# Kernel optimization log

Hardware: AMD Instinct MI355X
Metric: run time of the kernel (lower is better)

## Reference

```python
import jax, jax.numpy as jnp
import numpy as np

N_NODES = 20000
N_EDGES = 160000
N_GRAPHS = 64
IN_DIM = 1304  # 1280 + 24
NEG_SLOPE = 0.2


def gat_conv(x, src, dst, W, a_src, a_dst, b, heads, out_ch):
    """PyG-style GATConv (source_to_target flow, self loops already appended).
    x: [N, in], W: [in, heads*out], a_src/a_dst: [heads, out], b: [heads*out].
    Returns [N, heads*out] (concat=True)."""
    N = x.shape[0]
    h = (x @ W).reshape(N, heads, out_ch)                 # [N, H, C]
    e_src = jnp.sum(h * a_src[None], axis=-1)             # [N, H]
    e_dst = jnp.sum(h * a_dst[None], axis=-1)             # [N, H]
    e = jax.nn.leaky_relu(e_src[src] + e_dst[dst], NEG_SLOPE)  # [E, H]
    # softmax over incoming edges of each destination node
    e_max = jax.ops.segment_max(e, dst, num_segments=N)   # [N, H]
    e_exp = jnp.exp(e - e_max[dst])
    denom = jax.ops.segment_sum(e_exp, dst, num_segments=N)
    alpha = e_exp / (denom[dst] + 1e-16)                  # [E, H]
    msg = h[src] * alpha[:, :, None]                      # [E, H, C]
    out = jax.ops.segment_sum(msg, dst, num_segments=N)   # [N, H, C]
    return out.reshape(N, heads * out_ch) + b


def setup_inputs() -> dict:
    key = jax.random.key(0)
    ks = jax.random.split(key, 20)
    x = jax.random.normal(ks[0], (N_NODES, IN_DIM), dtype=jnp.float32)
    edge_index = jax.random.randint(ks[1], (2, N_EDGES), 0, N_NODES, dtype=jnp.int32)
    phy = jax.random.normal(ks[2], (N_GRAPHS, 188), dtype=jnp.float32)
    batch = jnp.sort(jax.random.randint(ks[3], (N_NODES,), 0, N_GRAPHS, dtype=jnp.int32))

    def glorot(k, shape):
        fan_in, fan_out = shape[0], shape[-1]
        lim = jnp.sqrt(6.0 / (fan_in + fan_out))
        return jax.random.uniform(k, shape, jnp.float32, -lim, lim)

    params = {
        # conv1: GATConv(1304, 256, heads=3)
        "W1": glorot(ks[4], (IN_DIM, 3 * 256)),
        "a_src1": glorot(ks[5], (3, 256)) * 0.1,
        "a_dst1": glorot(ks[6], (3, 256)) * 0.1,
        "b1": jnp.zeros((3 * 256,), jnp.float32),
        # conv2: GATConv(768, 256, heads=1)
        "W2": glorot(ks[7], (3 * 256, 256)),
        "a_src2": glorot(ks[8], (1, 256)) * 0.1,
        "a_dst2": glorot(ks[9], (1, 256)) * 0.1,
        "b2": jnp.zeros((256,), jnp.float32),
        # fc1
        "fc1_w1": glorot(ks[10], (188, 128)), "fc1_b1": jnp.zeros((128,), jnp.float32),
        "fc1_w2": glorot(ks[11], (128, 128)), "fc1_b2": jnp.zeros((128,), jnp.float32),
        # fc2
        "fc2_w1": glorot(ks[12], (256 + 128, 192)), "fc2_b1": jnp.zeros((192,), jnp.float32),
        "fc2_w2": glorot(ks[13], (192, 2)), "fc2_b2": jnp.zeros((2,), jnp.float32),
    }
    return {"x": x, "edge_index": edge_index, "phy": phy, "batch": batch, **params}


def reference(x, edge_index, phy, batch,
              W1, a_src1, a_dst1, b1,
              W2, a_src2, a_dst2, b2,
              fc1_w1, fc1_b1, fc1_w2, fc1_b2,
              fc2_w1, fc2_b1, fc2_w2, fc2_b2):
    N = x.shape[0]
    # add self loops (PyG GATConv default)
    loops = jnp.arange(N, dtype=edge_index.dtype)
    src = jnp.concatenate([edge_index[0], loops])
    dst = jnp.concatenate([edge_index[1], loops])

    h = gat_conv(x, src, dst, W1, a_src1, a_dst1, b1, heads=3, out_ch=256)
    h = jax.nn.relu(h)  # dropout is identity at inference
    h = gat_conv(h, src, dst, W2, a_src2, a_dst2, b2, heads=1, out_ch=256)

    # global mean pool per graph
    sums = jax.ops.segment_sum(h, batch, num_segments=N_GRAPHS)        # [B, 256]
    cnts = jax.ops.segment_sum(jnp.ones((N,), h.dtype), batch, num_segments=N_GRAPHS)
    pooled = sums / jnp.maximum(cnts, 1.0)[:, None]

    mid = jax.nn.relu(phy @ fc1_w1 + fc1_b1)
    mid = jax.nn.relu(mid @ fc1_w2 + fc1_b2)

    z = jnp.concatenate([pooled, mid], axis=1)                          # [B, 384]
    z = jax.nn.relu(z @ fc2_w1 + fc2_b1)
    logits = z @ fc2_w2 + fc2_b2
    return jax.nn.softmax(logits, axis=1)
```

## Files before the change

### kernel.cpp

```cpp
#include <hip/hip_runtime.h>
#include <hip/hip_bf16.h>
#include <math.h>

#define NN    20000
#define MP1   20224
#define NP    20096
#define E0    160000
#define EL    180000
#define NG    64
#define INDIM 1304
#define K1P   1344
#define GNT   21
#define GNX   3
#define GMB   79
#define NWG1  (GMB * GNX)
#define FB    ((EL + 511) / 512)
#define NEG_SLOPE 0.2f
#define NSB   20
#define PCH   32

#define ZB    80
#define XB    13272
#define WB    4800

typedef __bf16 bf16x8 __attribute__((ext_vector_type(8)));
typedef __bf16 bf16x4 __attribute__((ext_vector_type(4)));
typedef float  f32x4  __attribute__((ext_vector_type(4)));

__device__ __forceinline__ void gload16(const void* g, void* l) {
    __builtin_amdgcn_global_load_lds(
        (const __attribute__((address_space(1))) void*)g,
        (__attribute__((address_space(3))) void*)l, 16, 0, 0);
}

#define BAR()  { __builtin_amdgcn_s_barrier(); asm volatile("" ::: "memory"); }
#define VMW(n) { asm volatile("s_waitcnt vmcnt(" #n ")" ::: "memory"); __builtin_amdgcn_sched_barrier(0); }

__global__ __launch_bounds__(256)
void init_kernel(uint4* __restrict__ zreg, int n16,
                 const float* __restrict__ X, __hip_bfloat16* __restrict__ Xb,
                 const float* __restrict__ W1, const float* __restrict__ W2,
                 __hip_bfloat16* __restrict__ w1t, __hip_bfloat16* __restrict__ w2t) {
    const int b = blockIdx.x, t = threadIdx.x;
    if (b < ZB) {
        int i = b * 256 + t;
        if (i < n16) zreg[i] = (uint4){0u, 0u, 0u, 0u};
        return;
    }
    if (b < ZB + XB) {
        int idx = (b - ZB) * 256 + t;
        const int nb = K1P / 8;
        int row = idx / nb;
        int cb = (idx - row * nb) * 8;
        union { __hip_bfloat16 h[8]; float4 f4; } u;
        if (row < NN && cb + 8 <= INDIM) {
            const float4* p = (const float4*)(X + (size_t)row * INDIM + cb);
            float4 u0 = p[0], u1 = p[1];
            u.h[0] = __float2bfloat16(u0.x); u.h[1] = __float2bfloat16(u0.y);
            u.h[2] = __float2bfloat16(u0.z); u.h[3] = __float2bfloat16(u0.w);
            u.h[4] = __float2bfloat16(u1.x); u.h[5] = __float2bfloat16(u1.y);
            u.h[6] = __float2bfloat16(u1.z); u.h[7] = __float2bfloat16(u1.w);
        } else {
#pragma unroll
            for (int e = 0; e < 8; e++) {
                float f = (row < NN && cb + e < INDIM) ? X[(size_t)row * INDIM + cb + e] : 0.f;
                u.h[e] = __float2bfloat16(f);
            }
        }
        *(float4*)(Xb + (size_t)row * K1P + cb) = u.f4;
        return;
    }
    {
        int idx = (b - ZB - XB) * 256 + t;
        const int n1 = 768 * K1P;
        if (idx < n1) {
            int n = idx / K1P, k = idx - n * K1P;
            float f = (k < INDIM) ? W1[(size_t)k * 768 + n] : 0.f;
            w1t[idx] = __float2bfloat16(f);
        } else {
            int i2 = idx - n1;
            if (i2 < 256 * 768) {
                int n = i2 / 768, k = i2 - n * 768;
                w2t[i2] = __float2bfloat16(W2[(size_t)k * 256 + n]);
            }
        }
    }
}

__device__ __forceinline__ void stA(const __hip_bfloat16* __restrict__ A, int bm, int kt, int mh,
                                    char* abuf, int w, int l) {
#pragma unroll
    for (int u = 0; u < 2; u++) {
        int rl = (w << 3) + (l >> 3);
        int lrow = u * 128 + mh * 64 + rl;
        int skb = ((l & 7) << 4) ^ ((rl & 7) << 4);
        const char* g = (const char*)(A + (size_t)(bm + lrow) * K1P + kt * 64) + skb;
        gload16(g, abuf + (u * 128 + mh * 64) * 128 + (w << 10));
    }
}

__device__ __forceinline__ void stB(const __hip_bfloat16* __restrict__ Bt, int bn, int kt, int nh,
                                    char* bbuf, int w, int l) {
#pragma unroll
    for (int u = 0; u < 2; u++) {
        int c = u * 2 + (w >> 2);
        int row0 = c * 64 + nh * 32;
        int rl = ((w & 3) << 3) + (l >> 3);
        int skb = ((l & 7) << 4) ^ ((rl & 7) << 4);
        const char* g = (const char*)(Bt + (size_t)(bn + row0 + rl) * K1P + kt * 64) + skb;
        gload16(g, bbuf + row0 * 128 + ((w & 3) << 10));
    }
}

__global__ __launch_bounds__(512)
void gemm256(const __hip_bfloat16* __restrict__ A,
             const __hip_bfloat16* __restrict__ Bt,
             __hip_bfloat16* __restrict__ C,
             const float* __restrict__ a_src, const float* __restrict__ a_dst,
             float* __restrict__ esrc, float* __restrict__ edst, int M,
             const int* __restrict__ ei, const int* __restrict__ off,
             int* __restrict__ cur, int* __restrict__ csr) {
    __shared__ char lds[131072];
    const int t = threadIdx.x;

    if (blockIdx.x >= NWG1) {
        int e = (blockIdx.x - NWG1) * 512 + t;
        if (e < EL) {
            int d = (e < E0) ? ei[E0 + e] : (e - E0);
            int s = (e < E0) ? ei[e] : (e - E0);
            int pos = off[d] + atomicAdd(&cur[d], 1);
            csr[pos] = s;
        }
        return;
    }

    const int w = t >> 6, l = t & 63;
    const int wm = w >> 2, wn = w & 3;
    const int fr = l & 15, fq = l >> 4;
    const int amask = (fr & 7) << 4;

    const int nwg = NWG1;
    const int q8 = nwg >> 3, r8 = nwg & 7;
    const int xcd = blockIdx.x & 7, sub = blockIdx.x >> 3;
    const int logical = (xcd < r8 ? xcd * (q8 + 1) : r8 * (q8 + 1) + (xcd - r8) * q8) + sub;
    const int bm = (logical / GNX) * 256;
    const int bn = (logical % GNX) * 256;

    f32x4 acc[8][4];
#pragma unroll
    for (int i = 0; i < 8; i++)
#pragma unroll
        for (int j = 0; j < 4; j++) acc[i][j] = (f32x4){0.f, 0.f, 0.f, 0.f};

    char* A0 = lds;            char* B0 = lds + 32768;
    char* A1 = lds + 65536;    char* B1 = lds + 98304;

    stA(A, bm, 0, 0, A0, w, l);
    stB(Bt, bn, 0, 0, B0, w, l);
    stA(A, bm, 0, 1, A0, w, l);
    stB(Bt, bn, 0, 1, B0, w, l);
    stA(A, bm, 1, 0, A1, w, l);
    stB(Bt, bn, 1, 0, B1, w, l);
    VMW(8);
    BAR();

    for (int kt = 0; kt < GNT; kt++) {
        char* Ab = lds + (kt & 1) * 65536;
        char* Bb = Ab + 32768;
        char* An = lds + ((kt + 1) & 1) * 65536;
        char* Bn = An + 32768;
        bf16x8 a_c[4][2], b_c0[2][2], b_c1[2][2];

#pragma unroll
        for (int im = 0; im < 4; im++)
#pragma unroll
            for (int kk = 0; kk < 2; kk++)
                a_c[im][kk] = *(const bf16x8*)(Ab + (wm * 128 + im * 16 + fr) * 128 + ((kk * 64 + fq * 16) ^ amask));
#pragma unroll
        for (int jn = 0; jn < 2; jn++)
#pragma unroll
            for (int kk = 0; kk < 2; kk++)
                b_c0[jn][kk] = *(const bf16x8*)(Bb + (wn * 64 + jn * 16 + fr) * 128 + ((kk * 64 + fq * 16) ^ amask));
        if (kt + 1 < GNT) stA(A, bm, kt + 1, 1, An, w, l);
        BAR();
        __builtin_amdgcn_s_setprio(1);
#pragma unroll
        for (int im = 0; im < 4; im++)
#pragma unroll
            for (int jn = 0; jn < 2; jn++)
#pragma unroll
                for (int kk = 0; kk < 2; kk++)
                    acc[im][jn] = __builtin_amdgcn_mfma_f32_16x16x32_bf16(a_c[im][kk], b_c0[jn][kk], acc[im][jn], 0, 0, 0);
        __builtin_amdgcn_s_setprio(0);
        if (kt == GNT - 1) { VMW(0); } else { VMW(6); }
        BAR();

#pragma unroll
        for (int jn = 0; jn < 2; jn++)
#pragma unroll
            for (int kk = 0; kk < 2; kk++)
                b_c1[jn][kk] = *(const bf16x8*)(Bb + (wn * 64 + 32 + jn * 16 + fr) * 128 + ((kk * 64 + fq * 16) ^ amask));
        if (kt + 1 < GNT) stB(Bt, bn, kt + 1, 1, Bn, w, l);
        BAR();
        __builtin_amdgcn_s_setprio(1);
#pragma unroll
        for (int im = 0; im < 4; im++)
#pragma unroll
            for (int jn = 0; jn < 2; jn++)
#pragma unroll
                for (int kk = 0; kk < 2; kk++)
                    acc[im][2 + jn] = __builtin_amdgcn_mfma_f32_16x16x32_bf16(a_c[im][kk], b_c1[jn][kk], acc[im][2 + jn], 0, 0, 0);
        __builtin_amdgcn_s_setprio(0);
        if (kt == GNT - 1) { VMW(2); } else { VMW(10); }
        BAR();

#pragma unroll
        for (int im = 0; im < 4; im++)
#pragma unroll
            for (int kk = 0; kk < 2; kk++)
                a_c[im][kk] = *(const bf16x8*)(Ab + (wm * 128 + 64 + im * 16 + fr) * 128 + ((kk * 64 + fq * 16) ^ amask));
        if (kt + 2 < GNT) stA(A, bm, kt + 2, 0, Ab, w, l);
        BAR();
        __builtin_amdgcn_s_setprio(1);
#pragma unroll
        for (int im = 0; im < 4; im++)
#pragma unroll
            for (int jn = 0; jn < 2; jn++)
#pragma unroll
                for (int kk = 0; kk < 2; kk++)
                    acc[4 + im][jn] = __builtin_amdgcn_mfma_f32_16x16x32_bf16(a_c[im][kk], b_c0[jn][kk], acc[4 + im][jn], 0, 0, 0);
        __builtin_amdgcn_s_setprio(0);
        BAR();

        if (kt + 2 < GNT) stB(Bt, bn, kt + 2, 0, Bb, w, l);
        BAR();
        __builtin_amdgcn_s_setprio(1);
#pragma unroll
        for (int im = 0; im < 4; im++)
#pragma unroll
            for (int jn = 0; jn < 2; jn++)
#pragma unroll
                for (int kk = 0; kk < 2; kk++)
                    acc[4 + im][2 + jn] = __builtin_amdgcn_mfma_f32_16x16x32_bf16(a_c[im][kk], b_c1[jn][kk], acc[4 + im][2 + jn], 0, 0, 0);
        __builtin_amdgcn_s_setprio(0);
        if (kt + 2 < GNT) { VMW(8); }
        else if (kt + 2 == GNT) { VMW(4); }
        BAR();
    }

#pragma unroll
    for (int i = 0; i < 8; i++)
#pragma unroll
        for (int j = 0; j < 4; j++)
#pragma unroll
            for (int r = 0; r < 4; r++) {
                int row = bm + wm * 128 + i * 16 + fq * 4 + r;
                int col = bn + wn * 64 + j * 16 + fr;
                if (row < M) C[(size_t)row * 768 + col] = __float2bfloat16(acc[i][j][r]);
            }

    const int head = bn >> 8;
    float asv[4], adv[4];
#pragma unroll
    for (int j = 0; j < 4; j++) {
        asv[j] = a_src[head * 256 + wn * 64 + j * 16 + fr];
        adv[j] = a_dst[head * 256 + wn * 64 + j * 16 + fr];
    }
    __syncthreads();
    float* eb = (float*)lds;
#pragma unroll
    for (int i = 0; i < 8; i++) {
#pragma unroll
        for (int r = 0; r < 4; r++) {
            float ps = 0.f, pd = 0.f;
#pragma unroll
            for (int j = 0; j < 4; j++) { ps += acc[i][j][r] * asv[j]; pd += acc[i][j][r] * adv[j]; }
#pragma unroll
            for (int o = 8; o >= 1; o >>= 1) { ps += __shfl_xor(ps, o, 64); pd += __shfl_xor(pd, o, 64); }
            if (fr == 0) {
                int rowl = wm * 128 + i * 16 + fq * 4 + r;
                eb[(rowl * 4 + wn) * 2 + 0] = ps;
                eb[(rowl * 4 + wn) * 2 + 1] = pd;
            }
        }
    }
    __syncthreads();
    if (t < 256) {
        int row = bm + t;
        if (row < M) {
            float s = eb[t * 8 + 0] + eb[t * 8 + 2] + eb[t * 8 + 4] + eb[t * 8 + 6];
            float d = eb[t * 8 + 1] + eb[t * 8 + 3] + eb[t * 8 + 5] + eb[t * 8 + 7];
            esrc[row * 3 + head] = s;
            edst[row * 3 + head] = d;
        }
    }
}

__global__ __launch_bounds__(256)
void gemm2_fused(const __hip_bfloat16* __restrict__ A,
                 const __hip_bfloat16* __restrict__ Bt,
                 __hip_bfloat16* __restrict__ C,
                 const float* __restrict__ a_src2, const float* __restrict__ a_dst2,
                 float* __restrict__ esrc, float* __restrict__ edst,
                 int M, int N, int K, int NX) {
    __shared__ __hip_bfloat16 As[2][128 * 32];
    __shared__ __hip_bfloat16 Bs[2][128 * 32];
    const int t = threadIdx.x;
    const int w = t >> 6;
    const int l = t & 63;

    const int nwg = gridDim.x;
    const int q = nwg >> 3, r = nwg & 7;
    const int xcd = blockIdx.x & 7, idx = blockIdx.x >> 3;
    const int logical = (xcd < r ? xcd * (q + 1) : r * (q + 1) + (xcd - r) * q) + idx;
    const int bm = (logical / NX) * 128;
    const int bn = (logical % NX) * 128;

    const int wm = (w >> 1) * 64;
    const int wn = (w & 1) * 64;

    f32x4 acc[4][4];
#pragma unroll
    for (int i = 0; i < 4; i++)
#pragma unroll
        for (int j = 0; j < 4; j++) acc[i][j] = (f32x4){0.f, 0.f, 0.f, 0.f};

    const int sr = t >> 2;
    const int sc = (t & 3) * 8;
    const __hip_bfloat16* a0 = A  + (size_t)(bm + sr)      * K + sc;
    const __hip_bfloat16* a1 = A  + (size_t)(bm + 64 + sr) * K + sc;
    const __hip_bfloat16* b0 = Bt + (size_t)(bn + sr)      * K + sc;
    const __hip_bfloat16* b1 = Bt + (size_t)(bn + 64 + sr) * K + sc;

    const int fr = l & 15;
    const int fq = l >> 4;
    const int NT = K / 32;

    auto stage = [&](int k0, int b) {
        char* asb = (char*)&As[b][0];
        char* bsb = (char*)&Bs[b][0];
        gload16(a0 + k0, asb + w * 1024);
        gload16(a1 + k0, asb + 4096 + w * 1024);
        gload16(b0 + k0, bsb + w * 1024);
        gload16(b1 + k0, bsb + 4096 + w * 1024);
    };

    stage(0, 0);
    __syncthreads();

    for (int kt = 0; kt < NT; kt++) {
        const int cb = kt & 1;
        if (kt + 1 < NT) stage((kt + 1) * 32, cb ^ 1);
        bf16x8 av[4], bv[4];
#pragma unroll
        for (int i = 0; i < 4; i++)
            av[i] = *(const bf16x8*)&As[cb][(wm + i * 16 + fr) * 32 + fq * 8];
#pragma unroll
        for (int j = 0; j < 4; j++)
            bv[j] = *(const bf16x8*)&Bs[cb][(wn + j * 16 + fr) * 32 + fq * 8];
#pragma unroll
        for (int i = 0; i < 4; i++)
#pragma unroll
            for (int j = 0; j < 4; j++)
                acc[i][j] = __builtin_amdgcn_mfma_f32_16x16x32_bf16(av[i], bv[j], acc[i][j], 0, 0, 0);
        __syncthreads();
    }

#pragma unroll
    for (int i = 0; i < 4; i++) {
#pragma unroll
        for (int j = 0; j < 4; j++) {
#pragma unroll
            for (int r2 = 0; r2 < 4; r2++) {
                int row = bm + wm + i * 16 + fq * 4 + r2;
                int col = bn + wn + j * 16 + fr;
                if (row < M) C[(size_t)row * N + col] = __float2bfloat16(acc[i][j][r2]);
            }
        }
    }

    float asv[4], adv[4];
#pragma unroll
    for (int j = 0; j < 4; j++) {
        asv[j] = a_src2[bn + wn + j * 16 + fr];
        adv[j] = a_dst2[bn + wn + j * 16 + fr];
    }
    __syncthreads();
    float* eb = (float*)&As[0][0];
#pragma unroll
    for (int i = 0; i < 4; i++) {
#pragma unroll
        for (int r2 = 0; r2 < 4; r2++) {
            float ps = 0.f, pd = 0.f;
#pragma unroll
            for (int j = 0; j < 4; j++) { ps += acc[i][j][r2] * asv[j]; pd += acc[i][j][r2] * adv[j]; }
#pragma unroll
            for (int o = 8; o >= 1; o >>= 1) { ps += __shfl_xor(ps, o, 64); pd += __shfl_xor(pd, o, 64); }
            if (fr == 0) {
                int rowl = wm + i * 16 + fq * 4 + r2;
                int wnIdx = wn >> 6;
                eb[(rowl * 2 + wnIdx) * 2 + 0] = ps;
                eb[(rowl * 2 + wnIdx) * 2 + 1] = pd;
            }
        }
    }
    __syncthreads();
    if (t < 128) {
        int row = bm + t;
        if (row < M) {
            atomicAdd(&esrc[row], eb[t * 4 + 0] + eb[t * 4 + 2]);
            atomicAdd(&edst[row], eb[t * 4 + 1] + eb[t * 4 + 3]);
        }
    }
}

__global__ void hist_kernel(const int* __restrict__ ei, int* __restrict__ deg) {
    int e = blockIdx.x * 256 + threadIdx.x;
    if (e >= EL) return;
    int d = (e < E0) ? ei[E0 + e] : (e - E0);
    atomicAdd(&deg[d], 1);
}

__global__ __launch_bounds__(1024)
void scan_blk(const int* __restrict__ deg, int* __restrict__ off, int* __restrict__ bsum) {
    __shared__ int wsum[16];
    const int b = blockIdx.x, t = threadIdx.x, lane = t & 63, wv = t >> 6;
    const int i = b * 1024 + t;
    int v = (i < NN) ? deg[i] : 0;
    int x = v;
#pragma unroll
    for (int o = 1; o < 64; o <<= 1) {
        int y = __shfl_up(x, o, 64);
        if (lane >= o) x += y;
    }
    if (lane == 63) wsum[wv] = x;
    __syncthreads();
    if (wv == 0 && lane < 16) {
        int s = wsum[lane];
#pragma unroll
        for (int o = 1; o < 16; o <<= 1) {
            int y = __shfl_up(s, o, 64);
            if (lane >= o) s += y;
        }
        wsum[lane] = s;
    }
    __syncthreads();
    int woff = (wv == 0) ? 0 : wsum[wv - 1];
    if (i < NN) off[i + 1] = woff + x;
    if (t == 1023) bsum[b] = wsum[15];
}

__global__ __launch_bounds__(1024)
void scan_add(int* __restrict__ off, const int* __restrict__ bsum) {
    __shared__ int boffs[NSB];
    const int b = blockIdx.x, t = threadIdx.x;
    if (t < 64) {
        int lane = t;
        int v = (lane < NSB) ? bsum[lane] : 0;
        int x = v;
#pragma unroll
        for (int o = 1; o < 64; o <<= 1) {
            int y = __shfl_up(x, o, 64);
            if (lane >= o) x += y;
        }
        if (lane < NSB) boffs[lane] = x - v;
    }
    __syncthreads();
    const int i = b * 1024 + t;
    if (i < NN) off[i + 1] += boffs[b];
    if (b == 0 && t == 0) off[0] = 0;
}

template<int H, bool RELU, typename OutT>
__global__ __launch_bounds__(256)
void gat_aggregate(const __hip_bfloat16* __restrict__ hfeat,
                   const float* __restrict__ esrc,
                   const float* __restrict__ edst,
                   const int* __restrict__ off, const int* __restrict__ csr,
                   const float* __restrict__ bias,
                   OutT* __restrict__ out, int N) {
    const int wv = threadIdx.x >> 6, lane = threadIdx.x & 63;
    const int n = blockIdx.x * 4 + wv;
    if (n >= N) return;
    const int beg = off[n];
    const int deg = off[n + 1] - beg;

    float ed[H], m[H], den[H];
    f32x4 acc[H];
#pragma unroll
    for (int h = 0; h < H; h++) {
        ed[h] = edst[n * H + h];
        m[h] = -INFINITY;
        den[h] = 0.f;
        acc[h] = (f32x4){0.f, 0.f, 0.f, 0.f};
    }

    for (int base = 0; base < deg; base += 64) {
        const int i = base + lane;
        int s = 0;
        float lg[H];
        if (i < deg) {
            s = csr[beg + i];
#pragma unroll
            for (int h = 0; h < H; h++) {
                float v = esrc[s * H + h] + ed[h];
                lg[h] = (v >= 0.f) ? v : NEG_SLOPE * v;
            }
        } else {
#pragma unroll
            for (int h = 0; h < H; h++) lg[h] = -INFINITY;
        }
        float cm[H];
#pragma unroll
        for (int h = 0; h < H; h++) {
            cm[h] = lg[h];
#pragma unroll
            for (int o = 1; o < 64; o <<= 1)
                cm[h] = fmaxf(cm[h], __shfl_xor(cm[h], o, 64));
        }
#pragma unroll
        for (int h = 0; h < H; h++) {
            float nm = fmaxf(m[h], cm[h]);
            float sc = expf(m[h] - nm);
            den[h] *= sc;
#pragma unroll
            for (int e = 0; e < 4; e++) acc[h][e] *= sc;
            m[h] = nm;
        }
        float wgt[H];
#pragma unroll
        for (int h = 0; h < H; h++) {
            wgt[h] = (i < deg) ? expf(lg[h] - m[h]) : 0.f;
            den[h] += wgt[h];
        }
        const int cnt = min(64, deg - base);
        for (int j = 0; j < cnt; j++) {
            int sj = __shfl(s, j, 64);
#pragma unroll
            for (int h = 0; h < H; h++) {
                float wj = __shfl(wgt[h], j, 64);
                bf16x4 hv = *(const bf16x4*)(hfeat + (size_t)sj * (H * 256) + h * 256 + 4 * lane);
#pragma unroll
                for (int e = 0; e < 4; e++) acc[h][e] += wj * (float)hv[e];
            }
        }
    }
#pragma unroll
    for (int h = 0; h < H; h++) {
#pragma unroll
        for (int o = 1; o < 64; o <<= 1) den[h] += __shfl_xor(den[h], o, 64);
    }
#pragma unroll
    for (int h = 0; h < H; h++) {
        float inv = 1.f / (den[h] + 1e-16f);
        if constexpr (sizeof(OutT) == 2) {
            bf16x4 r;
#pragma unroll
            for (int e = 0; e < 4; e++) {
                float f = acc[h][e] * inv + bias[h * 256 + 4 * lane + e];
                if (RELU) f = fmaxf(f, 0.f);
                r[e] = (__bf16)f;
            }
            *(bf16x4*)((__hip_bfloat16*)out + (size_t)n * (H * 256) + h * 256 + 4 * lane) = r;
        } else {
            float4 r;
            float* rp = &r.x;
#pragma unroll
            for (int e = 0; e < 4; e++) {
                float f = acc[h][e] * inv + bias[h * 256 + 4 * lane + e];
                if (RELU) f = fmaxf(f, 0.f);
                rp[e] = f;
            }
            *(float4*)((float*)out + (size_t)n * (H * 256) + h * 256 + 4 * lane) = r;
        }
    }
}

__device__ __forceinline__ int lower_bound_batch(const int* __restrict__ batch, int key) {
    int lo = 0, hi = NN;
    while (lo < hi) {
        int mid = (lo + hi) >> 1;
        if (batch[mid] < key) lo = mid + 1; else hi = mid;
    }
    return lo;
}

__global__ __launch_bounds__(256)
void pool_partial(const __hip_bfloat16* __restrict__ out2, const int* __restrict__ batch,
                  float* __restrict__ partial, float* __restrict__ cnts) {
    const int g = blockIdx.x, c = blockIdx.y, t = threadIdx.x;
    const int s = lower_bound_batch(batch, g);
    const int e = lower_bound_batch(batch, g + 1);
    float a0 = 0.f, a1 = 0.f, a2 = 0.f, a3 = 0.f;
    int n = s + c;
    for (; n + 3 * PCH < e; n += 4 * PCH) {
        float v0 = __bfloat162float(out2[(size_t)n * 256 + t]);
        float v1 = __bfloat162float(out2[(size_t)(n + PCH) * 256 + t]);
        float v2 = __bfloat162float(out2[(size_t)(n + 2 * PCH) * 256 + t]);
        float v3 = __bfloat162float(out2[(size_t)(n + 3 * PCH) * 256 + t]);
        a0 += v0; a1 += v1; a2 += v2; a3 += v3;
    }
    for (; n < e; n += PCH) a0 += __bfloat162float(out2[(size_t)n * 256 + t]);
    partial[((size_t)g * PCH + c) * 256 + t] = a0 + a1 + a2 + a3;
    if (t == 0 && c == 0) cnts[g] = (float)(e - s);
}

__global__ __launch_bounds__(256)
void head_kernel(const float* __restrict__ partial, const float* __restrict__ cnts,
                 const float* __restrict__ phy,
                 const float* __restrict__ w11, const float* __restrict__ b11,
                 const float* __restrict__ w12, const float* __restrict__ b12,
                 const float* __restrict__ w21, const float* __restrict__ b21,
                 const float* __restrict__ w22, const float* __restrict__ b22,
                 float* __restrict__ out) {
    int g = blockIdx.x, t = threadIdx.x;
    __shared__ float ph[188];
    __shared__ float z[384];
    __shared__ float mid[128];
    __shared__ float t1[192];
    __shared__ float lg[2];
    if (t < 188) ph[t] = phy[g * 188 + t];
    {
        float s = 0.f;
#pragma unroll
        for (int c = 0; c < PCH; c++) s += partial[((size_t)g * PCH + c) * 256 + t];
        z[t] = s / fmaxf(cnts[g], 1.0f);
    }
    __syncthreads();
    if (t < 128) {
        float sm = b11[t];
        for (int k = 0; k < 188; k++) sm += ph[k] * w11[k * 128 + t];
        mid[t] = fmaxf(sm, 0.f);
    }
    __syncthreads();
    if (t < 128) {
        float sm = b12[t];
        for (int k = 0; k < 128; k++) sm += mid[k] * w12[k * 128 + t];
        z[256 + t] = fmaxf(sm, 0.f);
    }
    __syncthreads();
    if (t < 192) {
        float sm = b21[t];
        for (int k = 0; k < 384; k++) sm += z[k] * w21[k * 192 + t];
        t1[t] = fmaxf(sm, 0.f);
    }
    __syncthreads();
    if (t < 2) {
        float sm = b22[t];
        for (int k = 0; k < 192; k++) sm += t1[k] * w22[k * 2 + t];
        lg[t] = sm;
    }
    __syncthreads();
    if (t == 0) {
        float mx = fmaxf(lg[0], lg[1]);
        float e0 = expf(lg[0] - mx), e1 = expf(lg[1] - mx);
        float d = e0 + e1;
        out[g * 2 + 0] = e0 / d;
        out[g * 2 + 1] = e1 / d;
    }
}

extern "C" void kernel_launch(void* const* d_in, const int* in_sizes, int n_in,
                              void* d_out, int out_size, void* d_ws, size_t ws_size,
                              hipStream_t stream) {
    const float* x       = (const float*)d_in[0];
    const int*   ei      = (const int*)  d_in[1];
    const float* phy     = (const float*)d_in[2];
    const int*   batch   = (const int*)  d_in[3];
    const float* W1      = (const float*)d_in[4];
    const float* a_src1  = (const float*)d_in[5];
    const float* a_dst1  = (const float*)d_in[6];
    const float* b1      = (const float*)d_in[7];
    const float* W2      = (const float*)d_in[8];
    const float* a_src2  = (const float*)d_in[9];
    const float* a_dst2  = (const float*)d_in[10];
    const float* b2      = (const float*)d_in[11];
    const float* fc1_w1  = (const float*)d_in[12];
    const float* fc1_b1  = (const float*)d_in[13];
    const float* fc1_w2  = (const float*)d_in[14];
    const float* fc1_b2  = (const float*)d_in[15];
    const float* fc2_w1  = (const float*)d_in[16];
    const float* fc2_b1  = (const float*)d_in[17];
    const float* fc2_w2  = (const float*)d_in[18];
    const float* fc2_b2  = (const float*)d_in[19];
    float* out = (float*)d_out;

    char* base = (char*)d_ws;
    size_t o = 0;
    auto alloc = [&](size_t bytes) { size_t r = o; o += (bytes + 255) & ~255ULL; return r; };

    size_t o_xb   = alloc((size_t)MP1 * K1P * 2);
    size_t o_w1t  = alloc((size_t)768 * K1P * 2);
    size_t o_w2t  = alloc((size_t)256 * 768 * 2);
    size_t o_h1b  = alloc((size_t)NP * 768 * 2);
    size_t o_hob  = alloc((size_t)NP * 768 * 2);
    size_t o_es1  = alloc((size_t)NN * 3 * 4);
    size_t o_ed1  = alloc((size_t)NN * 3 * 4);
    size_t o_es2  = alloc((size_t)NN * 4);
    size_t o_ed2  = alloc((size_t)NN * 4);
    size_t o_deg  = alloc((size_t)(NN + 1) * 4);
    size_t o_cur  = alloc((size_t)NN * 4);
    size_t o_zend = o;
    size_t o_off  = alloc((size_t)(NN + 1) * 4);
    size_t o_csr  = alloc((size_t)EL * 4);
    size_t o_bsum = alloc((size_t)NSB * 4);
    size_t o_part = alloc((size_t)NG * PCH * 256 * 4);
    size_t o_cnts = alloc((size_t)NG * 4);

    __hip_bfloat16* xb   = (__hip_bfloat16*)(base + o_xb);
    __hip_bfloat16* w1t  = (__hip_bfloat16*)(base + o_w1t);
    __hip_bfloat16* w2t  = (__hip_bfloat16*)(base + o_w2t);
    __hip_bfloat16* h1b  = (__hip_bfloat16*)(base + o_h1b);
    __hip_bfloat16* hob  = (__hip_bfloat16*)(base + o_hob);
    __hip_bfloat16* h2b  = (__hip_bfloat16*)(base + o_xb);
    __hip_bfloat16* out2 = (__hip_bfloat16*)(base + o_xb + (size_t)24 * 1024 * 1024);
    float* es1   = (float*)(base + o_es1);
    float* ed1   = (float*)(base + o_ed1);
    float* es2   = (float*)(base + o_es2);
    float* ed2   = (float*)(base + o_ed2);
    int*   deg   = (int*)(base + o_deg);
    int*   cur   = (int*)(base + o_cur);
    int*   offs  = (int*)(base + o_off);
    int*   csr   = (int*)(base + o_csr);
    int*   bsum  = (int*)(base + o_bsum);
    float* part  = (float*)(base + o_part);
    float* cnts  = (float*)(base + o_cnts);

    {
        int n16 = (int)((o_zend - o_es2) / 16);
        init_kernel<<<ZB + XB + WB, 256, 0, stream>>>((uint4*)(base + o_es2), n16,
                                                      x, xb, W1, W2, w1t, w2t);
    }

    hist_kernel<<<(EL + 255) / 256, 256, 0, stream>>>(ei, deg);
    scan_blk<<<NSB, 1024, 0, stream>>>(deg, offs, bsum);
    scan_add<<<NSB, 1024, 0, stream>>>(offs, bsum);

    gemm256<<<NWG1 + FB, 512, 0, stream>>>(xb, w1t, h1b, a_src1, a_dst1, es1, ed1, NN,
                                           ei, offs, cur, csr);
    gat_aggregate<3, true, __hip_bfloat16><<<(NN + 3) / 4, 256, 0, stream>>>(h1b, es1, ed1, offs, csr, b1, hob, NN);

    gemm2_fused<<<2 * 157, 256, 0, stream>>>(hob, w2t, h2b, a_src2, a_dst2, es2, ed2, NN, 256, 768, 2);
    gat_aggregate<1, false, __hip_bfloat16><<<(NN + 3) / 4, 256, 0, stream>>>(h2b, es2, ed2, offs, csr, b2, out2, NN);

    pool_partial<<<dim3(NG, PCH), 256, 0, stream>>>(out2, batch, part, cnts);
    head_kernel<<<NG, 256, 0, stream>>>(part, cnts, phy,
                                        fc1_w1, fc1_b1, fc1_w2, fc1_b2,
                                        fc2_w1, fc2_b1, fc2_w2, fc2_b2, out);
}
```

Measured before the change: 234.6 us.

## Split GAT aggregation across heads and shrink CSR fill blocks to grid-stride

The aggregation kernel now gives each wavefront one (node, head) pair instead of one node handling all heads, so the first layer launches three times as many waves. Each wave carries less register state and the per-head gather chains become independent, which should improve latency hiding. The trade-off is that the CSR index loads, the softmax reductions and the pair division are now repeated once per head. Separately, the CSR fill blocks appended to the first GEMM drop from about 352 to 19 and use a grid-stride loop, so fewer extra workgroups compete with the GEMM tiles.

```diff
diff --git a/kernel.cpp b/kernel.cpp
--- a/kernel.cpp
+++ b/kernel.cpp
@@ -14,7 +14,7 @@
 #define GNX   3
 #define GMB   79
 #define NWG1  (GMB * GNX)
-#define FB    ((EL + 511) / 512)
+#define FB    19
 #define NEG_SLOPE 0.2f
 #define NSB   20
 #define PCH   32
@@ -124,8 +124,7 @@
     const int t = threadIdx.x;
 
     if (blockIdx.x >= NWG1) {
-        int e = (blockIdx.x - NWG1) * 512 + t;
-        if (e < EL) {
+        for (int e = (blockIdx.x - NWG1) * 512 + t; e < EL; e += FB * 512) {
             int d = (e < E0) ? ei[E0 + e] : (e - E0);
             int s = (e < E0) ? ei[e] : (e - E0);
             int pos = off[d] + atomicAdd(&cur[d], 1);
@@ -480,99 +479,70 @@
                    const float* __restrict__ bias,
                    OutT* __restrict__ out, int N) {
     const int wv = threadIdx.x >> 6, lane = threadIdx.x & 63;
-    const int n = blockIdx.x * 4 + wv;
-    if (n >= N) return;
+    const int pair = blockIdx.x * 4 + wv;
+    if (pair >= N * H) return;
+    const int n = pair / H;
+    const int h = pair - n * H;
     const int beg = off[n];
     const int deg = off[n + 1] - beg;
 
-    float ed[H], m[H], den[H];
-    f32x4 acc[H];
-#pragma unroll
-    for (int h = 0; h < H; h++) {
-        ed[h] = edst[n * H + h];
-        m[h] = -INFINITY;
-        den[h] = 0.f;
-        acc[h] = (f32x4){0.f, 0.f, 0.f, 0.f};
-    }
+    const float ed = edst[n * H + h];
+    float m = -INFINITY, den = 0.f;
+    f32x4 acc = (f32x4){0.f, 0.f, 0.f, 0.f};
 
     for (int base = 0; base < deg; base += 64) {
         const int i = base + lane;
         int s = 0;
-        float lg[H];
+        float lg = -INFINITY;
         if (i < deg) {
             s = csr[beg + i];
-#pragma unroll
-            for (int h = 0; h < H; h++) {
-                float v = esrc[s * H + h] + ed[h];
-                lg[h] = (v >= 0.f) ? v : NEG_SLOPE * v;
-            }
-        } else {
-#pragma unroll
-            for (int h = 0; h < H; h++) lg[h] = -INFINITY;
-        }
-        float cm[H];
-#pragma unroll
-        for (int h = 0; h < H; h++) {
-            cm[h] = lg[h];
-#pragma unroll
-            for (int o = 1; o < 64; o <<= 1)
-                cm[h] = fmaxf(cm[h], __shfl_xor(cm[h], o, 64));
-        }
-#pragma unroll
-        for (int h = 0; h < H; h++) {
-            float nm = fmaxf(m[h], cm[h]);
-            float sc = expf(m[h] - nm);
-            den[h] *= sc;
-#pragma unroll
-            for (int e = 0; e < 4; e++) acc[h][e] *= sc;
-            m[h] = nm;
-        }
-        float wgt[H];
-#pragma unroll
-        for (int h = 0; h < H; h++) {
-            wgt[h] = (i < deg) ? expf(lg[h] - m[h]) : 0.f;
-            den[h] += wgt[h];
-        }
+            float v = esrc[s * H + h] + ed;
+            lg = (v >= 0.f) ? v : NEG_SLOPE * v;
+        }
+        float cm = lg;
+#pragma unroll
+        for (int o = 1; o < 64; o <<= 1)
+            cm = fmaxf(cm, __shfl_xor(cm, o, 64));
+        float nm = fmaxf(m, cm);
+        float sc = expf(m - nm);
+        den *= sc;
+#pragma unroll
+        for (int e = 0; e < 4; e++) acc[e] *= sc;
+        m = nm;
+        float wgt = (i < deg) ? expf(lg - m) : 0.f;
+        den += wgt;
         const int cnt = min(64, deg - base);
         for (int j = 0; j < cnt; j++) {
             int sj = __shfl(s, j, 64);
-#pragma unroll
-            for (int h = 0; h < H; h++) {
-                float wj = __shfl(wgt[h], j, 64);
-                bf16x4 hv = *(const bf16x4*)(hfeat + (size_t)sj * (H * 256) + h * 256 + 4 * lane);
-#pragma unroll
-                for (int e = 0; e < 4; e++) acc[h][e] += wj * (float)hv[e];
-            }
-        }
-    }
-#pragma unroll
-    for (int h = 0; h < H; h++) {
-#pragma unroll
-        for (int o = 1; o < 64; o <<= 1) den[h] += __shfl_xor(den[h], o, 64);
-    }
-#pragma unroll
-    for (int h = 0; h < H; h++) {
-        float inv = 1.f / (den[h] + 1e-16f);
-        if constexpr (sizeof(OutT) == 2) {
-            bf16x4 r;
-#pragma unroll
-            for (int e = 0; e < 4; e++) {
-                float f = acc[h][e] * inv + bias[h * 256 + 4 * lane + e];
-                if (RELU) f = fmaxf(f, 0.f);
-                r[e] = (__bf16)f;
-            }
-            *(bf16x4*)((__hip_bfloat16*)out + (size_t)n * (H * 256) + h * 256 + 4 * lane) = r;
-        } else {
-            float4 r;
-            float* rp = &r.x;
-#pragma unroll
-            for (int e = 0; e < 4; e++) {
-                float f = acc[h][e] * inv + bias[h * 256 + 4 * lane + e];
-                if (RELU) f = fmaxf(f, 0.f);
-                rp[e] = f;
-            }
-            *(float4*)((float*)out + (size_t)n * (H * 256) + h * 256 + 4 * lane) = r;
-        }
+            float wj = __shfl(wgt, j, 64);
+            bf16x4 hv = *(const bf16x4*)(hfeat + (size_t)sj * (H * 256) + h * 256 + 4 * lane);
+#pragma unroll
+            for (int e = 0; e < 4; e++) acc[e] += wj * (float)hv[e];
+        }
+    }
+#pragma unroll
+    for (int o = 1; o < 64; o <<= 1) den += __shfl_xor(den, o, 64);
+
+    float inv = 1.f / (den + 1e-16f);
+    if constexpr (sizeof(OutT) == 2) {
+        bf16x4 r;
+#pragma unroll
+        for (int e = 0; e < 4; e++) {
+            float f = acc[e] * inv + bias[h * 256 + 4 * lane + e];
+            if (RELU) f = fmaxf(f, 0.f);
+            r[e] = (__bf16)f;
+        }
+        *(bf16x4*)((__hip_bfloat16*)out + (size_t)n * (H * 256) + h * 256 + 4 * lane) = r;
+    } else {
+        float4 r;
+        float* rp = &r.x;
+#pragma unroll
+        for (int e = 0; e < 4; e++) {
+            float f = acc[e] * inv + bias[h * 256 + 4 * lane + e];
+            if (RELU) f = fmaxf(f, 0.f);
+            rp[e] = f;
+        }
+        *(float4*)((float*)out + (size_t)n * (H * 256) + h * 256 + 4 * lane) = r;
     }
 }
 
@@ -738,7 +708,7 @@
 
     gemm256<<<NWG1 + FB, 512, 0, stream>>>(xb, w1t, h1b, a_src1, a_dst1, es1, ed1, NN,
                                            ei, offs, cur, csr);
-    gat_aggregate<3, true, __hip_bfloat16><<<(NN + 3) / 4, 256, 0, stream>>>(h1b, es1, ed1, offs, csr, b1, hob, NN);
+    gat_aggregate<3, true, __hip_bfloat16><<<(NN * 3 + 3) / 4, 256, 0, stream>>>(h1b, es1, ed1, offs, csr, b1, hob, NN);
 
     gemm2_fused<<<2 * 157, 256, 0, stream>>>(hob, w2t, h2b, a_src2, a_dst2, es2, ed2, NN, 256, 768, 2);
     gat_aggregate<1, false, __hip_bfloat16><<<(NN + 3) / 4, 256, 0, stream>>>(h2b, es2, ed2, offs, csr, b2, out2, NN);
```

Measured after the change: 232.9 us. About the same (-0.7%).
